# Performance work log

Measured on AMD Instinct MI355X. Metric: run time of the kernel, lower is better.

The kernel has to match this reference:

```python
import jax, jax.numpy as jnp
import numpy as np

D = 512
H = 8
HD = D // H
EPS = 1e-5
NEG_INF = -1e30


def _ln(x, g, b):
    mu = jnp.mean(x, axis=-1, keepdims=True)
    var = jnp.mean(jnp.square(x - mu), axis=-1, keepdims=True)
    return (x - mu) * jax.lax.rsqrt(var + EPS) * g + b


def setup_inputs() -> dict:
    key = jax.random.key(0)
    ks = jax.random.split(key, 8)
    V, M, S = 128, 128, 514  # seq includes 2 head tokens (cls+dist)
    inp = {
        "video_embeds": jax.random.normal(ks[0], (V, D), jnp.float32),
        "music_features": jax.random.normal(ks[1], (M, S, D), jnp.float32),
        "music_masks": jnp.ones((M, S - 2), jnp.int32),
    }
    wk = jax.random.split(ks[2], 5)
    for name, k in zip(["Wq", "Wk", "Wv", "Wo", "Wl"], wk):
        inp[name] = jax.random.normal(k, (D, D), jnp.float32) * 0.02
    for name in ["bq", "bk", "bv", "bo", "bl"]:
        inp[name] = jnp.zeros((D,), jnp.float32)
    for name in ["g1", "g2", "g3"]:
        inp[name] = jnp.ones((D,), jnp.float32)
    for name in ["b1", "b2", "b3"]:
        inp[name] = jnp.zeros((D,), jnp.float32)
    return inp


def reference(video_embeds, music_features, music_masks,
              Wq, bq, Wk, bk, Wv, bv, Wo, bo, Wl, bl,
              g1, b1, g2, b2, g3, b3):
    # drop cls + dist tokens
    mf = music_features[:, 2:, :]  # (M, f, D)
    ve = _ln(video_embeds, g1, b1)  # (V, D)
    mf = _ln(mf, g1, b1)
    V = ve.shape[0]
    M, f, _ = mf.shape

    q = (ve @ Wq.T + bq).reshape(V, H, HD).transpose(1, 0, 2)        # (H, V, hd)
    k = (mf @ Wk.T + bk).reshape(M, f, H, HD).transpose(0, 2, 1, 3)  # (M, H, f, hd)
    v = (mf @ Wv.T + bv).reshape(M, f, H, HD).transpose(0, 2, 1, 3)  # (M, H, f, hd)

    logits = jnp.einsum('hvd,mhfd->vmhf', q, k) / np.sqrt(HD).astype(np.float32)
    mask = music_masks[None, :, None, :]  # (1, M, 1, f)
    logits = jnp.where(mask == 0, NEG_INF, logits)
    w = jax.nn.softmax(logits, axis=-1)
    attn = jnp.einsum('vmhf,mhfd->vmhd', w, v).reshape(V, M, D)
    attn = attn @ Wo.T + bo

    attn = _ln(attn, g2, b2)
    out = attn + (attn @ Wl.T + bl)  # dropout = identity in eval
    return _ln(out, g3, b3)
```

## Files before the change

kernel.cpp:

```cpp
#include <hip/hip_runtime.h>
#include <hip/hip_bf16.h>

typedef unsigned int uint;
typedef unsigned short ushort;
typedef __bf16 bf16;
typedef bf16 bf16x8 __attribute__((ext_vector_type(8)));
typedef float f32x4 __attribute__((ext_vector_type(4)));
typedef ushort ushort4v __attribute__((ext_vector_type(4)));

__device__ __forceinline__ float bf2f(ushort u) {
  union { uint u; float f; } v; v.u = ((uint)u) << 16; return v.f;
}
__device__ __forceinline__ ushort f2bf(float f) {
  union { float f; uint u; } v; v.f = f;
  uint u = v.u;
  uint r = (u + 0x7fffu + ((u >> 16) & 1u)) >> 16;
  return (ushort)r;
}

__device__ __forceinline__ void gl2lds16(const void* g, void* l) {
  __builtin_amdgcn_global_load_lds(
      (const __attribute__((address_space(1))) void*)g,
      (__attribute__((address_space(3))) void*)l, 16, 0, 0);
}

struct CastArgs {
  const float* s0; const float* s1; const float* s2; const float* s3; const float* s4;
  ushort* d0; ushort* d1; ushort* d2; ushort* d3; ushort* d4;
};
__global__ __launch_bounds__(256) void bfcast5(CastArgs a) {
  int t = blockIdx.x * 256 + threadIdx.x;
  int which = t >> 15;
  int e = (t & 32767) * 8;
  const float* s = which == 0 ? a.s0 : which == 1 ? a.s1 : which == 2 ? a.s2 : which == 3 ? a.s3 : a.s4;
  ushort*      d = which == 0 ? a.d0 : which == 1 ? a.d1 : which == 2 ? a.d2 : which == 3 ? a.d3 : a.d4;
  float4 v0 = *(const float4*)(s + e);
  float4 v1 = *(const float4*)(s + e + 4);
  uint4 o;
  o.x = (uint)f2bf(v0.x) | ((uint)f2bf(v0.y) << 16);
  o.y = (uint)f2bf(v0.z) | ((uint)f2bf(v0.w) << 16);
  o.z = (uint)f2bf(v1.x) | ((uint)f2bf(v1.y) << 16);
  o.w = (uint)f2bf(v1.z) | ((uint)f2bf(v1.w) << 16);
  *(uint4*)(d + e) = o;
}

__global__ __launch_bounds__(256) void ln512v(
    int mode, int nrows,
    const void* __restrict__ srcA, const void* __restrict__ srcB,
    const float* __restrict__ g, const float* __restrict__ b,
    void* __restrict__ dst)
{
  const int l = threadIdx.x & 63;
  const int nw = gridDim.x * 4;
  for (int row = blockIdx.x * 4 + (threadIdx.x >> 6); row < nrows; row += nw) {
    float x[8];
    if (mode <= 1) {
      const float* s;
      if (mode == 0) {
        s = (const float*)srcA + (size_t)row * 512;
      } else {
        int mm = row >> 9, fi = row & 511;
        s = (const float*)srcA + ((size_t)mm * 514 + 2 + fi) * 512;
      }
      float4 a0 = *(const float4*)(s + l * 4);
      float4 a1 = *(const float4*)(s + 256 + l * 4);
      x[0] = a0.x; x[1] = a0.y; x[2] = a0.z; x[3] = a0.w;
      x[4] = a1.x; x[5] = a1.y; x[6] = a1.z; x[7] = a1.w;
    } else if (mode == 2) {
      const ushort* s = (const ushort*)srcA + (size_t)row * 512;
      uint4 u = *(const uint4*)(s + l * 8);
      x[0] = bf2f((ushort)u.x); x[1] = bf2f((ushort)(u.x >> 16));
      x[2] = bf2f((ushort)u.y); x[3] = bf2f((ushort)(u.y >> 16));
      x[4] = bf2f((ushort)u.z); x[5] = bf2f((ushort)(u.z >> 16));
      x[6] = bf2f((ushort)u.w); x[7] = bf2f((ushort)(u.w >> 16));
    } else {
      const ushort* sa = (const ushort*)srcA + (size_t)row * 512;
      const ushort* sb = (const ushort*)srcB + (size_t)row * 512;
      uint4 ua = *(const uint4*)(sa + l * 8);
      uint4 ub = *(const uint4*)(sb + l * 8);
      x[0] = bf2f((ushort)ua.x) + bf2f((ushort)ub.x);
      x[1] = bf2f((ushort)(ua.x >> 16)) + bf2f((ushort)(ub.x >> 16));
      x[2] = bf2f((ushort)ua.y) + bf2f((ushort)ub.y);
      x[3] = bf2f((ushort)(ua.y >> 16)) + bf2f((ushort)(ub.y >> 16));
      x[4] = bf2f((ushort)ua.z) + bf2f((ushort)ub.z);
      x[5] = bf2f((ushort)(ua.z >> 16)) + bf2f((ushort)(ub.z >> 16));
      x[6] = bf2f((ushort)ua.w) + bf2f((ushort)ub.w);
      x[7] = bf2f((ushort)(ua.w >> 16)) + bf2f((ushort)(ub.w >> 16));
    }
    float sum = 0.f, sq = 0.f;
    #pragma unroll
    for (int j = 0; j < 8; ++j) { sum += x[j]; sq += x[j] * x[j]; }
    #pragma unroll
    for (int o = 1; o < 64; o <<= 1) {
      sum += __shfl_xor(sum, o);
      sq  += __shfl_xor(sq, o);
    }
    const float inv = 1.f / 512.f;
    float mu = sum * inv;
    float var = sq * inv - mu * mu;
    float rstd = rsqrtf(var + 1e-5f);

    float gv[8], bv[8];
    if (mode <= 1) {
      float4 g0 = *(const float4*)(g + l * 4);
      float4 g1 = *(const float4*)(g + 256 + l * 4);
      float4 b0 = *(const float4*)(b + l * 4);
      float4 b1 = *(const float4*)(b + 256 + l * 4);
      gv[0] = g0.x; gv[1] = g0.y; gv[2] = g0.z; gv[3] = g0.w;
      gv[4] = g1.x; gv[5] = g1.y; gv[6] = g1.z; gv[7] = g1.w;
      bv[0] = b0.x; bv[1] = b0.y; bv[2] = b0.z; bv[3] = b0.w;
      bv[4] = b1.x; bv[5] = b1.y; bv[6] = b1.z; bv[7] = b1.w;
    } else {
      float4 g0 = *(const float4*)(g + l * 8);
      float4 g1 = *(const float4*)(g + l * 8 + 4);
      float4 b0 = *(const float4*)(b + l * 8);
      float4 b1 = *(const float4*)(b + l * 8 + 4);
      gv[0] = g0.x; gv[1] = g0.y; gv[2] = g0.z; gv[3] = g0.w;
      gv[4] = g1.x; gv[5] = g1.y; gv[6] = g1.z; gv[7] = g1.w;
      bv[0] = b0.x; bv[1] = b0.y; bv[2] = b0.z; bv[3] = b0.w;
      bv[4] = b1.x; bv[5] = b1.y; bv[6] = b1.z; bv[7] = b1.w;
    }
    float y[8];
    #pragma unroll
    for (int j = 0; j < 8; ++j) y[j] = (x[j] - mu) * rstd * gv[j] + bv[j];

    if (mode <= 1) {
      ushort* d = (ushort*)dst + (size_t)row * 512;
      ushort4v p0, p1;
      #pragma unroll
      for (int j = 0; j < 4; ++j) { p0[j] = f2bf(y[j]); p1[j] = f2bf(y[4 + j]); }
      *(ushort4v*)(d + l * 4) = p0;
      *(ushort4v*)(d + 256 + l * 4) = p1;
    } else if (mode == 2) {
      ushort* d = (ushort*)dst + (size_t)row * 512;
      uint4 o;
      o.x = (uint)f2bf(y[0]) | ((uint)f2bf(y[1]) << 16);
      o.y = (uint)f2bf(y[2]) | ((uint)f2bf(y[3]) << 16);
      o.z = (uint)f2bf(y[4]) | ((uint)f2bf(y[5]) << 16);
      o.w = (uint)f2bf(y[6]) | ((uint)f2bf(y[7]) << 16);
      *(uint4*)(d + l * 8) = o;
    } else {
      float* d = (float*)dst + (size_t)row * 512;
      float4 o0, o1;
      o0.x = y[0]; o0.y = y[1]; o0.z = y[2]; o0.w = y[3];
      o1.x = y[4]; o1.y = y[5]; o1.z = y[6]; o1.w = y[7];
      *(float4*)(d + l * 8) = o0;
      *(float4*)(d + l * 8 + 4) = o1;
    }
  }
}

__global__ __launch_bounds__(256) void gemm512(
    const ushort* __restrict__ A, const ushort* __restrict__ W,
    const float* __restrict__ bias, ushort* __restrict__ C,
    float scale, int vt_mode)
{
  __shared__ __align__(16) ushort As[128 * 64];
  __shared__ __align__(16) ushort Bs[128 * 64];
  const int tid = threadIdx.x;
  const int w = tid >> 6, l = tid & 63;
  const int lg = l >> 4, lr = l & 15;
  const int wr = w >> 1, wc = w & 1;
  const int row0 = blockIdx.y * 128, col0 = blockIdx.x * 128;

  f32x4 acc[4][4];
  #pragma unroll
  for (int i = 0; i < 4; i++)
    #pragma unroll
    for (int j = 0; j < 4; j++) { f32x4 z = {0.f,0.f,0.f,0.f}; acc[i][j] = z; }

  for (int kk = 0; kk < 8; ++kk) {
    #pragma unroll
    for (int c2 = 0; c2 < 4; ++c2) {
      int c = c2 * 256 + tid;
      int r = c >> 3, j = c & 7;
      int ksrc = kk * 64 + ((j * 8) ^ ((r & 7) * 8));
      gl2lds16(A + (size_t)(row0 + r) * 512 + ksrc, As + (c2 * 256 + w * 64) * 8);
      gl2lds16(W + (size_t)(col0 + r) * 512 + ksrc, Bs + (c2 * 256 + w * 64) * 8);
    }
    __syncthreads();
    #pragma unroll
    for (int k2 = 0; k2 < 2; ++k2) {
      bf16x8 af[4], bfr[4];
      #pragma unroll
      for (int mi = 0; mi < 4; ++mi) {
        int r = wr * 64 + mi * 16 + lr;
        af[mi] = *(const bf16x8*)(As + r * 64 + ((k2 * 32 + lg * 8) ^ ((r & 7) * 8)));
      }
      #pragma unroll
      for (int ni = 0; ni < 4; ++ni) {
        int r = wc * 64 + ni * 16 + lr;
        bfr[ni] = *(const bf16x8*)(Bs + r * 64 + ((k2 * 32 + lg * 8) ^ ((r & 7) * 8)));
      }
      #pragma unroll
      for (int mi = 0; mi < 4; ++mi)
        #pragma unroll
        for (int ni = 0; ni < 4; ++ni)
          acc[mi][ni] = __builtin_amdgcn_mfma_f32_16x16x32_bf16(af[mi], bfr[ni], acc[mi][ni], 0, 0, 0);
    }
    __syncthreads();
  }

  #pragma unroll
  for (int ni = 0; ni < 4; ++ni) {
    int cg = col0 + wc * 64 + ni * 16 + lr;
    float bc = bias[cg];
    #pragma unroll
    for (int mi = 0; mi < 4; ++mi) {
      int rg0 = row0 + wr * 64 + mi * 16 + lg * 4;
      if (!vt_mode) {
        #pragma unroll
        for (int e = 0; e < 4; ++e) {
          float v = (acc[mi][ni][e] + bc) * scale;
          C[(size_t)(rg0 + e) * 512 + cg] = f2bf(v);
        }
      } else {
        int m = rg0 >> 9, fi = rg0 & 511;
        ushort4v pk;
        #pragma unroll
        for (int e = 0; e < 4; ++e) pk[e] = f2bf((acc[mi][ni][e] + bc) * scale);
        *(ushort4v*)(C + (size_t)(m * 512 + cg) * 512 + fi) = pk;
      }
    }
  }
}

__global__ __launch_bounds__(256) void attn_kernel(
    const ushort* __restrict__ q, const ushort* __restrict__ k,
    const ushort* __restrict__ vt, const int* __restrict__ masks,
    ushort* __restrict__ attn)
{
  __shared__ __align__(16) ushort Qs[128 * 64];
  __shared__ __align__(16) ushort Ks[64 * 64];
  __shared__ __align__(16) ushort Vs[64 * 64];
  __shared__ __align__(16) ushort Ps[4][32 * 64];
  __shared__ float maskf[64];
  __shared__ float stats[4][32];

  const int tid = threadIdx.x;
  const int w = tid >> 6, l = tid & 63;
  const int lg = l >> 4, lr = l & 15;
  const int m = blockIdx.x >> 3, h = blockIdx.x & 7;

  const size_t kbase = (size_t)(m * 512) * 512 + h * 64;
  const size_t vbase = (size_t)(m * 512 + h * 64) * 512;

  #pragma unroll
  for (int c2 = 0; c2 < 4; ++c2) {
    int c = c2 * 256 + tid;
    int r = c >> 3, j = c & 7;
    gl2lds16(q + (size_t)r * 512 + h * 64 + ((j * 8) ^ ((r & 7) * 8)),
             Qs + (c2 * 256 + w * 64) * 8);
  }

  f32x4 acc[2][4];
  #pragma unroll
  for (int i = 0; i < 2; i++)
    #pragma unroll
    for (int j = 0; j < 4; j++) { f32x4 z = {0.f,0.f,0.f,0.f}; acc[i][j] = z; }
  float m_run[2] = {-INFINITY, -INFINITY};
  float l_run[2] = {0.f, 0.f};
  bf16x8 qf[2][2];

  for (int it = 0; it < 8; ++it) {
    const int f0 = it * 64;
    #pragma unroll
    for (int c2 = 0; c2 < 2; ++c2) {
      int c = c2 * 256 + tid;
      int r = c >> 3, j = c & 7;
      int off = (j * 8) ^ ((r & 7) * 8);
      gl2lds16(k + kbase + (size_t)(f0 + r) * 512 + off, Ks + (c2 * 256 + w * 64) * 8);
      gl2lds16(vt + vbase + (size_t)r * 512 + f0 + off, Vs + (c2 * 256 + w * 64) * 8);
    }
    if (tid < 64) maskf[tid] = masks[m * 512 + f0 + tid] ? 0.f : -1e30f;
    __syncthreads();

    if (it == 0) {
      #pragma unroll
      for (int nv = 0; nv < 2; ++nv)
        #pragma unroll
        for (int k2 = 0; k2 < 2; ++k2) {
          int v = w * 32 + nv * 16 + lr;
          qf[nv][k2] = *(const bf16x8*)(Qs + v * 64 + ((k2 * 32 + lg * 8) ^ ((v & 7) * 8)));
        }
    }

    f32x4 s[4][2];
    #pragma unroll
    for (int mi = 0; mi < 4; mi++)
      #pragma unroll
      for (int nv = 0; nv < 2; nv++) { f32x4 z = {0.f,0.f,0.f,0.f}; s[mi][nv] = z; }
    #pragma unroll
    for (int k2 = 0; k2 < 2; ++k2) {
      bf16x8 kf[4];
      #pragma unroll
      for (int mi = 0; mi < 4; ++mi) {
        int f = mi * 16 + lr;
        kf[mi] = *(const bf16x8*)(Ks + f * 64 + ((k2 * 32 + lg * 8) ^ ((f & 7) * 8)));
      }
      #pragma unroll
      for (int mi = 0; mi < 4; ++mi)
        #pragma unroll
        for (int nv = 0; nv < 2; ++nv)
          s[mi][nv] = __builtin_amdgcn_mfma_f32_16x16x32_bf16(kf[mi], qf[nv][k2], s[mi][nv], 0, 0, 0);
    }

    float mk[4][4];
    #pragma unroll
    for (int mi = 0; mi < 4; mi++)
      #pragma unroll
      for (int e = 0; e < 4; e++) mk[mi][e] = maskf[mi * 16 + lg * 4 + e];

    #pragma unroll
    for (int nv = 0; nv < 2; ++nv) {
      float cmax = -INFINITY;
      #pragma unroll
      for (int mi = 0; mi < 4; mi++)
        #pragma unroll
        for (int e = 0; e < 4; e++) {
          s[mi][nv][e] += mk[mi][e];
          cmax = fmaxf(cmax, s[mi][nv][e]);
        }
      cmax = fmaxf(cmax, __shfl_xor(cmax, 16));
      cmax = fmaxf(cmax, __shfl_xor(cmax, 32));
      float mnew = fmaxf(m_run[nv], cmax);
      float sc = __expf(m_run[nv] - mnew);
      float csum = 0.f;
      int vloc = nv * 16 + lr;
      #pragma unroll
      for (int mi = 0; mi < 4; mi++) {
        ushort4v pk;
        #pragma unroll
        for (int e = 0; e < 4; e++) {
          float p = __expf(s[mi][nv][e] - mnew);
          csum += p;
          pk[e] = f2bf(p);
        }
        int f = mi * 16 + lg * 4;
        *(ushort4v*)(&Ps[w][vloc * 64 + (f ^ ((vloc & 7) * 8))]) = pk;
      }
      csum += __shfl_xor(csum, 16);
      csum += __shfl_xor(csum, 32);
      l_run[nv] = l_run[nv] * sc + csum;
      m_run[nv] = mnew;
      if (lg == 0) stats[w][vloc] = sc;
    }

    #pragma unroll
    for (int mi2 = 0; mi2 < 2; ++mi2)
      #pragma unroll
      for (int e = 0; e < 4; ++e) {
        float sc = stats[w][mi2 * 16 + lg * 4 + e];
        #pragma unroll
        for (int nd = 0; nd < 4; ++nd) acc[mi2][nd][e] *= sc;
      }

    #pragma unroll
    for (int k2 = 0; k2 < 2; ++k2) {
      bf16x8 pf[2], vf[4];
      #pragma unroll
      for (int mi2 = 0; mi2 < 2; ++mi2) {
        int vloc = mi2 * 16 + lr;
        pf[mi2] = *(const bf16x8*)(&Ps[w][vloc * 64 + ((k2 * 32 + lg * 8) ^ ((vloc & 7) * 8))]);
      }
      #pragma unroll
      for (int nd = 0; nd < 4; ++nd) {
        int d = nd * 16 + lr;
        vf[nd] = *(const bf16x8*)(Vs + d * 64 + ((k2 * 32 + lg * 8) ^ ((d & 7) * 8)));
      }
      #pragma unroll
      for (int mi2 = 0; mi2 < 2; ++mi2)
        #pragma unroll
        for (int nd = 0; nd < 4; ++nd)
          acc[mi2][nd] = __builtin_amdgcn_mfma_f32_16x16x32_bf16(pf[mi2], vf[nd], acc[mi2][nd], 0, 0, 0);
    }
    __syncthreads();
  }

  #pragma unroll
  for (int nv = 0; nv < 2; ++nv)
    if (lg == 0) stats[w][nv * 16 + lr] = 1.f / l_run[nv];
  #pragma unroll
  for (int mi2 = 0; mi2 < 2; ++mi2)
    #pragma unroll
    for (int e = 0; e < 4; ++e) {
      float invl = stats[w][mi2 * 16 + lg * 4 + e];
      int vg = w * 32 + mi2 * 16 + lg * 4 + e;
      #pragma unroll
      for (int nd = 0; nd < 4; ++nd) {
        int d = nd * 16 + lr;
        attn[(size_t)(vg * 128 + m) * 512 + h * 64 + d] = f2bf(acc[mi2][nd][e] * invl);
      }
    }
}

extern "C" void kernel_launch(void* const* d_in, const int* in_sizes, int n_in,
                              void* d_out, int out_size, void* d_ws, size_t ws_size,
                              hipStream_t stream) {
  const float* video = (const float*)d_in[0];
  const float* music = (const float*)d_in[1];
  const int*   masks = (const int*)d_in[2];
  const float* Wq = (const float*)d_in[3];
  const float* Wk = (const float*)d_in[4];
  const float* Wv = (const float*)d_in[5];
  const float* Wo = (const float*)d_in[6];
  const float* Wl = (const float*)d_in[7];
  const float* bq = (const float*)d_in[8];
  const float* bk = (const float*)d_in[9];
  const float* bv = (const float*)d_in[10];
  const float* bo = (const float*)d_in[11];
  const float* bl = (const float*)d_in[12];
  const float* g1 = (const float*)d_in[13];
  const float* g2 = (const float*)d_in[14];
  const float* g3 = (const float*)d_in[15];
  const float* b1 = (const float*)d_in[16];
  const float* b2 = (const float*)d_in[17];
  const float* b3 = (const float*)d_in[18];

  char* ws = (char*)d_ws;
  ushort* mfln = (ushort*)(ws);
  ushort* kbuf = (ushort*)(ws + 67108864);
  ushort* vtb  = (ushort*)(ws + 134217728);
  ushort* attn = (ushort*)(ws + 201326592);
  ushort* c1   = (ushort*)(ws + 218103808);
  ushort* xbuf = (ushort*)(ws + 234881024);
  ushort* veln = (ushort*)(ws + 251658240);
  ushort* qbuf = (ushort*)(ws + 251789312);
  ushort* wqb  = (ushort*)(ws + 251920384);
  ushort* wkb  = wqb + 262144;
  ushort* wvb  = wkb + 262144;
  ushort* wob  = wvb + 262144;
  ushort* wlb  = wob + 262144;

  CastArgs ca = {Wq, Wk, Wv, Wo, Wl, wqb, wkb, wvb, wob, wlb};
  bfcast5<<<640, 256, 0, stream>>>(ca);

  ln512v<<<32, 256, 0, stream>>>(0, 128, video, nullptr, g1, b1, veln);
  ln512v<<<2048, 256, 0, stream>>>(1, 65536, music, nullptr, g1, b1, mfln);

  gemm512<<<dim3(4, 1), 256, 0, stream>>>(veln, wqb, bq, qbuf, 0.125f, 0);
  gemm512<<<dim3(4, 512), 256, 0, stream>>>(mfln, wkb, bk, kbuf, 1.f, 0);
  gemm512<<<dim3(4, 512), 256, 0, stream>>>(mfln, wvb, bv, vtb, 1.f, 1);

  attn_kernel<<<1024, 256, 0, stream>>>(qbuf, kbuf, vtb, masks, attn);

  gemm512<<<dim3(4, 128), 256, 0, stream>>>(attn, wob, bo, c1, 1.f, 0);
  ln512v<<<2048, 256, 0, stream>>>(2, 16384, c1, nullptr, g2, b2, xbuf);
  gemm512<<<dim3(4, 128), 256, 0, stream>>>(xbuf, wlb, bl, c1, 1.f, 0);
  ln512v<<<2048, 256, 0, stream>>>(3, 16384, xbuf, c1, g3, b3, d_out);
}
```

Baseline: 319.9 us.

## Widen GEMM tile to 128x256 with 512 threads and XCD-aware block remap

The projection GEMM now uses 512-thread blocks that each compute a 128x256 output tile, so every A tile loaded into LDS is reused across twice as many output columns. It also remaps block IDs into contiguous chunks, which appears aimed at spreading work across the MI355X's chiplets for better cache locality. The intent is to cut redundant global and LDS traffic for A. The cost is larger LDS use per block and half as many blocks, which may lower occupancy, and the tiny Q GEMM gets only two blocks.

```diff
diff --git a/kernel.cpp b/kernel.cpp
--- a/kernel.cpp
+++ b/kernel.cpp
@@ -150,18 +150,23 @@
   }
 }
 
-__global__ __launch_bounds__(256) void gemm512(
+__global__ __launch_bounds__(512) void gemm512x(
     const ushort* __restrict__ A, const ushort* __restrict__ W,
     const float* __restrict__ bias, ushort* __restrict__ C,
     float scale, int vt_mode)
 {
   __shared__ __align__(16) ushort As[128 * 64];
-  __shared__ __align__(16) ushort Bs[128 * 64];
+  __shared__ __align__(16) ushort Bs[256 * 64];
   const int tid = threadIdx.x;
   const int w = tid >> 6, l = tid & 63;
   const int lg = l >> 4, lr = l & 15;
-  const int wr = w >> 1, wc = w & 1;
-  const int row0 = blockIdx.y * 128, col0 = blockIdx.x * 128;
+  const int wr = w >> 2, wc = w & 3;
+
+  int nwg = gridDim.x * gridDim.y;
+  int bid = blockIdx.y * gridDim.x + blockIdx.x;
+  if ((nwg & 7) == 0) bid = (bid & 7) * (nwg >> 3) + (bid >> 3);
+  const int bx = bid % gridDim.x, by = bid / gridDim.x;
+  const int row0 = by * 128, col0 = bx * 256;
 
   f32x4 acc[4][4];
   #pragma unroll
@@ -171,26 +176,32 @@
 
   for (int kk = 0; kk < 8; ++kk) {
     #pragma unroll
-    for (int c2 = 0; c2 < 4; ++c2) {
-      int c = c2 * 256 + tid;
+    for (int li = 0; li < 2; ++li) {
+      int c = li * 512 + tid;
       int r = c >> 3, j = c & 7;
-      int ksrc = kk * 64 + ((j * 8) ^ ((r & 7) * 8));
-      gl2lds16(A + (size_t)(row0 + r) * 512 + ksrc, As + (c2 * 256 + w * 64) * 8);
-      gl2lds16(W + (size_t)(col0 + r) * 512 + ksrc, Bs + (c2 * 256 + w * 64) * 8);
+      gl2lds16(A + (size_t)(row0 + r) * 512 + kk * 64 + ((j ^ (r & 7)) * 8),
+               As + (li * 512 + w * 64) * 8);
+    }
+    #pragma unroll
+    for (int li = 0; li < 4; ++li) {
+      int c = li * 512 + tid;
+      int r = c >> 3, j = c & 7;
+      gl2lds16(W + (size_t)(col0 + r) * 512 + kk * 64 + ((j ^ (r & 7)) * 8),
+               Bs + (li * 512 + w * 64) * 8);
     }
     __syncthreads();
     #pragma unroll
-    for (int k2 = 0; k2 < 2; ++k2) {
+    for (int ks = 0; ks < 2; ++ks) {
       bf16x8 af[4], bfr[4];
       #pragma unroll
       for (int mi = 0; mi < 4; ++mi) {
         int r = wr * 64 + mi * 16 + lr;
-        af[mi] = *(const bf16x8*)(As + r * 64 + ((k2 * 32 + lg * 8) ^ ((r & 7) * 8)));
+        af[mi] = *(const bf16x8*)(As + r * 64 + ((ks * 32 + lg * 8) ^ ((r & 7) * 8)));
       }
       #pragma unroll
       for (int ni = 0; ni < 4; ++ni) {
         int r = wc * 64 + ni * 16 + lr;
-        bfr[ni] = *(const bf16x8*)(Bs + r * 64 + ((k2 * 32 + lg * 8) ^ ((r & 7) * 8)));
+        bfr[ni] = *(const bf16x8*)(Bs + r * 64 + ((ks * 32 + lg * 8) ^ ((r & 7) * 8)));
       }
       #pragma unroll
       for (int mi = 0; mi < 4; ++mi)
@@ -438,14 +449,14 @@
   ln512v<<<32, 256, 0, stream>>>(0, 128, video, nullptr, g1, b1, veln);
   ln512v<<<2048, 256, 0, stream>>>(1, 65536, music, nullptr, g1, b1, mfln);
 
-  gemm512<<<dim3(4, 1), 256, 0, stream>>>(veln, wqb, bq, qbuf, 0.125f, 0);
-  gemm512<<<dim3(4, 512), 256, 0, stream>>>(mfln, wkb, bk, kbuf, 1.f, 0);
-  gemm512<<<dim3(4, 512), 256, 0, stream>>>(mfln, wvb, bv, vtb, 1.f, 1);
+  gemm512x<<<dim3(2, 1), 512, 0, stream>>>(veln, wqb, bq, qbuf, 0.125f, 0);
+  gemm512x<<<dim3(2, 512), 512, 0, stream>>>(mfln, wkb, bk, kbuf, 1.f, 0);
+  gemm512x<<<dim3(2, 512), 512, 0, stream>>>(mfln, wvb, bv, vtb, 1.f, 1);
 
   attn_kernel<<<1024, 256, 0, stream>>>(qbuf, kbuf, vtb, masks, attn);
 
-  gemm512<<<dim3(4, 128), 256, 0, stream>>>(attn, wob, bo, c1, 1.f, 0);
+  gemm512x<<<dim3(2, 128), 512, 0, stream>>>(attn, wob, bo, c1, 1.f, 0);
   ln512v<<<2048, 256, 0, stream>>>(2, 16384, c1, nullptr, g2, b2, xbuf);
-  gemm512<<<dim3(4, 128), 256, 0, stream>>>(xbuf, wlb, bl, c1, 1.f, 0);
+  gemm512x<<<dim3(2, 128), 512, 0, stream>>>(xbuf, wlb, bl, c1, 1.f, 0);
   ln512v<<<2048, 256, 0, stream>>>(3, 16384, xbuf, c1, g3, b3, d_out);
 }
```

Result: faster. 309.3 us (-3.3%).
